# Kernel tuning notes

Measured on AMD Instinct MI355X. Metric: run time of the kernel, lower is better.

The kernel has to match this reference:

```python
import jax, jax.numpy as jnp
import numpy as np

B, S = 16, 4096
E_ENC, E_DEC, H = 1024, 1024, 512


def setup_inputs() -> dict:
    key = jax.random.key(0)
    ks = jax.random.split(key, 8)
    sc_e = 1.0 / np.sqrt(E_ENC)
    sc_d = 1.0 / np.sqrt(E_DEC)
    sc_h = 1.0 / np.sqrt(H)
    return {
        "encoder_hiddens": jax.random.normal(ks[0], (B, S, E_ENC), jnp.float32),
        "decoder_hidden": jax.random.normal(ks[1], (B, E_DEC), jnp.float32),
        "We": jax.random.uniform(ks[2], (E_ENC, H), jnp.float32, -sc_e, sc_e),
        "be": jax.random.uniform(ks[3], (H,), jnp.float32, -sc_e, sc_e),
        "Wd": jax.random.uniform(ks[4], (E_DEC, H), jnp.float32, -sc_d, sc_d),
        "bd": jax.random.uniform(ks[5], (H,), jnp.float32, -sc_d, sc_d),
        "Wo": jax.random.uniform(ks[6], (H, 1), jnp.float32, -sc_h, sc_h),
        "bo": jax.random.uniform(ks[7], (1,), jnp.float32, -sc_h, sc_h),
    }


def reference(encoder_hiddens, decoder_hidden, We, be, Wd, bd, Wo, bo):
    # Additive (Bahdanau) attention.
    # enc_proj: [B,S,H]; dec_proj: [B,1,H] broadcast over sequence.
    enc_proj = jnp.einsum("bse,eh->bsh", encoder_hiddens, We) + be
    dec_proj = jnp.einsum("bd,dh->bh", decoder_hidden, Wd) + bd
    e = jnp.tanh(enc_proj + dec_proj[:, None, :])          # [B,S,H]
    scores = jnp.einsum("bsh,h->bs", e, Wo[:, 0]) + bo[0]  # [B,S]
    attn = jax.nn.softmax(scores, axis=-1)                 # [B,S]
    context = jnp.einsum("bs,bse->be", attn, encoder_hiddens)  # [B,E_ENC]
    return context
```

## Files before the change

### kernel.cpp

```cpp
#include <hip/hip_runtime.h>
#include <hip/hip_bf16.h>
#include <math.h>

#define B_ 16
#define S_ 4096
#define E_ 1024
#define H_ 512

#define BM 128
#define BN 128
#define BK 64
#define NCHUNK (E_ / BK)

typedef short bf16x8 __attribute__((ext_vector_type(8)));
typedef unsigned short u16x8 __attribute__((ext_vector_type(8)));
typedef float f32x4 __attribute__((ext_vector_type(4)));

__device__ inline unsigned short f2bf(float x) {
    __hip_bfloat16 h = __float2bfloat16(x);
    return *(unsigned short*)&h;
}
__device__ inline float bf2f(unsigned short u) {
    unsigned int x = ((unsigned int)u) << 16;
    float f;
    __builtin_memcpy(&f, &x, 4);
    return f;
}
__device__ __forceinline__ void gld16(const unsigned short* g, unsigned short* l) {
    __builtin_amdgcn_global_load_lds(
        (const __attribute__((address_space(1))) void*)g,
        (__attribute__((address_space(3))) void*)l, 16, 0, 0);
}

__global__ __launch_bounds__(256) void prep_conv_kernel(
    const float* __restrict__ enc, const float* __restrict__ We,
    const float* __restrict__ dec, const float* __restrict__ Wd,
    const float* __restrict__ bd, const float* __restrict__ be,
    unsigned short* __restrict__ WeTcB, float* __restrict__ dp,
    unsigned short* __restrict__ encB) {
    __shared__ float red[4][64];
    int bid = blockIdx.x, t = threadIdx.x;
    if (bid < 64) {
        int c = bid >> 2, n0t = (bid & 3) * 128;
#pragma unroll 4
        for (int it = 0; it < 32; ++it) {
            int o = it * 256 + t;
            int n_rel = o >> 6, within = o & 63;
            int cp = within >> 3, j = within & 7;
            int n = n0t + n_rel;
            int k = c * 64 + ((cp ^ (n & 7)) << 3) + j;
            WeTcB[c * 32768 + n * 64 + within] = f2bf(We[(size_t)k * H_ + n]);
        }
    } else if (bid < 192) {
        int id = bid - 64;
        int b = id >> 3, hc = id & 7;
        int h = hc * 64 + (t & 63);
        int ec = t >> 6;
        const float* dr = dec + b * E_ + ec * 256;
        const float* wp = Wd + (size_t)(ec * 256) * H_ + h;
        float acc = 0.f;
#pragma unroll 8
        for (int e = 0; e < 256; ++e) acc = fmaf(dr[e], wp[(size_t)e * H_], acc);
        red[ec][t & 63] = acc;
        __syncthreads();
        if (t < 64) {
            int hh = hc * 64 + t;
            dp[b * H_ + hh] = red[0][t] + red[1][t] + red[2][t] + red[3][t] + bd[hh] + be[hh];
        }
    } else {
        size_t base = ((size_t)(bid - 192) * 256 + t) * 16;
        const float* ep = enc + base;
        unsigned short* op = encB + base;
        float4 v0 = *(const float4*)(ep);
        float4 v1 = *(const float4*)(ep + 4);
        float4 v2 = *(const float4*)(ep + 8);
        float4 v3 = *(const float4*)(ep + 12);
        u16x8 u0, u1;
        u0[0] = f2bf(v0.x); u0[1] = f2bf(v0.y); u0[2] = f2bf(v0.z); u0[3] = f2bf(v0.w);
        u0[4] = f2bf(v1.x); u0[5] = f2bf(v1.y); u0[6] = f2bf(v1.z); u0[7] = f2bf(v1.w);
        u1[0] = f2bf(v2.x); u1[1] = f2bf(v2.y); u1[2] = f2bf(v2.z); u1[3] = f2bf(v2.w);
        u1[4] = f2bf(v3.x); u1[5] = f2bf(v3.y); u1[6] = f2bf(v3.z); u1[7] = f2bf(v3.w);
        *(u16x8*)(op) = u0;
        *(u16x8*)(op + 8) = u1;
    }
}

__global__ __launch_bounds__(256, 3) void scores_gemm_kernel(
    const unsigned short* __restrict__ encB, const unsigned short* __restrict__ WeTcB,
    const float* __restrict__ Wo, const float* __restrict__ dp,
    float* __restrict__ parts) {
    __shared__ unsigned short sA[BM * BK];
    __shared__ unsigned short sB[BN * BK];
    __shared__ float sRed[2][BM];

    int tid = threadIdx.x;
    int w = tid >> 6, l = tid & 63;
    int l16 = l & 15, quad = l >> 4;
    int wm = w & 1, wn = w >> 1;
    int bid = blockIdx.x;
    int xcd = bid & 7;
    int sq = bid >> 3;
    int nt = sq & 3;
    size_t mt = (size_t)((sq >> 2) << 3) + xcd;
    size_t m0 = mt * BM;
    int n0 = nt * BN;
    int b = (int)(m0 >> 12);

    int lrow = l >> 3, lcp = l & 7;
    int qa = lcp ^ (lrow & 7);
    const unsigned short* gA = encB + (m0 + w * 8 + lrow) * E_ + qa * 8;
    const unsigned short* gB = WeTcB + (size_t)n0 * BK + (w * 8) * BK + l * 8;
    unsigned short* sAb = sA + (w * 8) * BK;
    unsigned short* sBb = sB + (w * 8) * BK;

    f32x4 acc[4][4];
#pragma unroll
    for (int i = 0; i < 4; ++i)
#pragma unroll
        for (int j = 0; j < 4; ++j) acc[i][j] = (f32x4)0.f;

    int arow = (wm * 64 + l16) * BK;
    int brow = (wn * 64 + l16) * BK;
    int sw = l16 & 7;

    for (int c = 0; c < NCHUNK; ++c) {
        __syncthreads();
        int k0 = c * BK;
#pragma unroll
        for (int i = 0; i < 4; ++i) {
            gld16(gA + (size_t)i * 32 * E_ + k0, sAb + i * 32 * BK);
            gld16(gB + (size_t)c * (H_ * BK) + i * 32 * BK, sBb + i * 32 * BK);
        }
        __syncthreads();
#pragma unroll
        for (int half = 0; half < 2; ++half) {
            int koff = (((half * 4 + quad) ^ sw) << 3);
            bf16x8 aR[4], bR[4];
#pragma unroll
            for (int i = 0; i < 4; ++i)
                aR[i] = *(const bf16x8*)(sA + arow + i * 16 * BK + koff);
#pragma unroll
            for (int j = 0; j < 4; ++j)
                bR[j] = *(const bf16x8*)(sB + brow + j * 16 * BK + koff);
#pragma unroll
            for (int i = 0; i < 4; ++i)
#pragma unroll
                for (int j = 0; j < 4; ++j)
                    acc[i][j] = __builtin_amdgcn_mfma_f32_16x16x32_bf16(aR[i], bR[j], acc[i][j], 0, 0, 0);
        }
    }

    float dpv[4], wov[4];
    const float* dpb = dp + b * H_;
#pragma unroll
    for (int j = 0; j < 4; ++j) {
        int h = n0 + wn * 64 + j * 16 + l16;
        dpv[j] = dpb[h];
        wov[j] = Wo[h];
    }
#pragma unroll
    for (int i = 0; i < 4; ++i)
#pragma unroll
        for (int r = 0; r < 4; ++r) {
            float s = 0.f;
#pragma unroll
            for (int j = 0; j < 4; ++j) {
                float x = acc[i][j][r] + dpv[j];
                float e = __expf(2.f * x);
                s += (1.f - 2.f / (e + 1.f)) * wov[j];
            }
            s += __shfl_xor(s, 1, 64);
            s += __shfl_xor(s, 2, 64);
            s += __shfl_xor(s, 4, 64);
            s += __shfl_xor(s, 8, 64);
            if (l16 == 0) sRed[wn][wm * 64 + i * 16 + quad * 4 + r] = s;
        }
    __syncthreads();
    if (tid < BM) {
        int s_in = (int)(m0 & (S_ - 1)) + tid;
        parts[(size_t)(nt * B_ + b) * S_ + s_in] = sRed[0][tid] + sRed[1][tid];
    }
}

__global__ __launch_bounds__(256) void stats_kernel(const float* __restrict__ parts,
                                                    float2* __restrict__ stats) {
    int b = blockIdx.x, tid = threadIdx.x;
    const float4* p0 = (const float4*)(parts + (size_t)(0 * B_ + b) * S_);
    const float4* p1 = (const float4*)(parts + (size_t)(1 * B_ + b) * S_);
    const float4* p2 = (const float4*)(parts + (size_t)(2 * B_ + b) * S_);
    const float4* p3 = (const float4*)(parts + (size_t)(3 * B_ + b) * S_);
    float4 v[4];
    float m = -1e30f;
#pragma unroll
    for (int i = 0; i < 4; ++i) {
        int idx = i * 256 + tid;
        float4 a0 = p0[idx], a1 = p1[idx], a2 = p2[idx], a3 = p3[idx];
        v[i].x = a0.x + a1.x + a2.x + a3.x;
        v[i].y = a0.y + a1.y + a2.y + a3.y;
        v[i].z = a0.z + a1.z + a2.z + a3.z;
        v[i].w = a0.w + a1.w + a2.w + a3.w;
        m = fmaxf(m, fmaxf(fmaxf(v[i].x, v[i].y), fmaxf(v[i].z, v[i].w)));
    }
    for (int off = 32; off; off >>= 1) m = fmaxf(m, __shfl_xor(m, off, 64));
    __shared__ float redm[4];
    __shared__ float reds[4];
    if ((tid & 63) == 0) redm[tid >> 6] = m;
    __syncthreads();
    m = fmaxf(fmaxf(redm[0], redm[1]), fmaxf(redm[2], redm[3]));
    float s = 0.f;
#pragma unroll
    for (int i = 0; i < 4; ++i) {
        s += __expf(v[i].x - m) + __expf(v[i].y - m);
        s += __expf(v[i].z - m) + __expf(v[i].w - m);
    }
    for (int off = 32; off; off >>= 1) s += __shfl_xor(s, off, 64);
    if ((tid & 63) == 0) reds[tid >> 6] = s;
    __syncthreads();
    if (tid == 0) {
        stats[b] = make_float2(m, reds[0] + reds[1] + reds[2] + reds[3]);
    }
}

__global__ __launch_bounds__(256) void ctx_partial_bf16(
    const unsigned short* __restrict__ encB, const float* __restrict__ parts,
    const float2* __restrict__ stats, float* __restrict__ part) {
    int b = blockIdx.x >> 5;
    int c = blockIdx.x & 31;
    int s0 = c * 128;
    int tid = threadIdx.x;
    __shared__ float w[128];
    if (tid < 128) {
        size_t idx = (size_t)b * S_ + s0 + tid;
        float x = parts[(size_t)(0 * B_) * S_ + idx] + parts[(size_t)(1 * B_) * S_ + idx] +
                  parts[(size_t)(2 * B_) * S_ + idx] + parts[(size_t)(3 * B_) * S_ + idx];
        w[tid] = __expf(x - stats[b].x);
    }
    __syncthreads();
    int e8 = (tid & 127) * 8;
    int sh = tid >> 7;
    const unsigned short* base = encB + ((size_t)b * S_ + s0 + sh * 64) * E_ + e8;
    const float* wp = w + sh * 64;
    float acc[8];
#pragma unroll
    for (int t = 0; t < 8; ++t) acc[t] = 0.f;
    for (int s = 0; s < 64; s += 8) {
        u16x8 v[8];
#pragma unroll
        for (int u = 0; u < 8; ++u) v[u] = *(const u16x8*)(base + (size_t)(s + u) * E_);
#pragma unroll
        for (int u = 0; u < 8; ++u) {
            float ws = wp[s + u];
#pragma unroll
            for (int t = 0; t < 8; ++t) acc[t] = fmaf(ws, bf2f(v[u][t]), acc[t]);
        }
    }
    float* po = part + ((size_t)(b * 64 + c * 2 + sh)) * E_ + e8;
    *(float4*)(po) = make_float4(acc[0], acc[1], acc[2], acc[3]);
    *(float4*)(po + 4) = make_float4(acc[4], acc[5], acc[6], acc[7]);
}

__global__ __launch_bounds__(256) void ctx_reduce(const float* __restrict__ part,
                                                  const float2* __restrict__ stats,
                                                  float* __restrict__ out) {
    int idx = blockIdx.x * 256 + threadIdx.x;
    int b = idx >> 10;
    int e = idx & 1023;
    const float* p = part + (size_t)b * 64 * E_ + e;
    float s0 = 0.f, s1 = 0.f, s2 = 0.f, s3 = 0.f;
    for (int c = 0; c < 64; c += 4) {
        s0 += p[(size_t)(c + 0) * E_];
        s1 += p[(size_t)(c + 1) * E_];
        s2 += p[(size_t)(c + 2) * E_];
        s3 += p[(size_t)(c + 3) * E_];
    }
    out[idx] = ((s0 + s1) + (s2 + s3)) * (1.f / stats[b].y);
}

extern "C" void kernel_launch(void* const* d_in, const int* in_sizes, int n_in,
                              void* d_out, int out_size, void* d_ws, size_t ws_size,
                              hipStream_t stream) {
    const float* enc = (const float*)d_in[0];
    const float* dec = (const float*)d_in[1];
    const float* We  = (const float*)d_in[2];
    const float* be  = (const float*)d_in[3];
    const float* Wd  = (const float*)d_in[4];
    const float* bd  = (const float*)d_in[5];
    const float* Wo  = (const float*)d_in[6];
    float* out = (float*)d_out;

    char* wsp = (char*)d_ws;
    unsigned short* WeTcB = (unsigned short*)wsp;
    float* dp = (float*)(wsp + (1 << 20));
    float2* stats = (float2*)(wsp + (1 << 20) + (32 << 10));
    float* parts = (float*)(wsp + (1 << 20) + (64 << 10));
    float* part = (float*)(wsp + (4 << 20));
    unsigned short* encB = (unsigned short*)(wsp + (8 << 20));

    prep_conv_kernel<<<192 + 16384, 256, 0, stream>>>(enc, We, dec, Wd, bd, be,
                                                      WeTcB, dp, encB);
    scores_gemm_kernel<<<(B_ * S_ / BM) * (H_ / BN), 256, 0, stream>>>(
        encB, WeTcB, Wo, dp, parts);
    stats_kernel<<<B_, 256, 0, stream>>>(parts, stats);
    ctx_partial_bf16<<<B_ * 32, 256, 0, stream>>>(encB, parts, stats, part);
    ctx_reduce<<<B_ * E_ / 256, 256, 0, stream>>>(part, stats, out);
}
```

Measured before the change: 485.9 us.

## Enlarge score GEMM tiles to 256x256 with double-buffered, staged LDS pipeline

The scores GEMM moves from 128x128 tiles with 4 waves to 256x256 tiles with 8 waves per block. LDS is double-buffered, and the A/B global-to-LDS loads for future K chunks are interleaved between MFMA phases, gated by explicit vmcnt waits, raw barriers and setprio. With 256-wide H tiles only two partial score planes remain, so the stats and context kernels now sum two partials instead of four. The aim is more data reuse per LDS byte and overlap of load latency with MFMA work. The cost is about 128KB of LDS per block, which limits occupancy, plus fragile hand-tuned wait counts.

```diff
diff --git a/kernel.cpp b/kernel.cpp
--- a/kernel.cpp
+++ b/kernel.cpp
@@ -7,8 +7,8 @@
 #define E_ 1024
 #define H_ 512
 
-#define BM 128
-#define BN 128
+#define BM 256
+#define BN 256
 #define BK 64
 #define NCHUNK (E_ / BK)
 
@@ -26,11 +26,14 @@
     __builtin_memcpy(&f, &x, 4);
     return f;
 }
-__device__ __forceinline__ void gld16(const unsigned short* g, unsigned short* l) {
-    __builtin_amdgcn_global_load_lds(
-        (const __attribute__((address_space(1))) void*)g,
-        (__attribute__((address_space(3))) void*)l, 16, 0, 0);
-}
+
+#define GLD16(g, l_) __builtin_amdgcn_global_load_lds(                     \
+    (const __attribute__((address_space(1))) void*)(g),                    \
+    (__attribute__((address_space(3))) void*)(l_), 16, 0, 0)
+
+#define BAR() do { asm volatile("" ::: "memory");                          \
+                   __builtin_amdgcn_s_barrier();                           \
+                   asm volatile("" ::: "memory"); } while (0)
 
 __global__ __launch_bounds__(256) void prep_conv_kernel(
     const float* __restrict__ enc, const float* __restrict__ We,
@@ -85,100 +88,178 @@
     }
 }
 
-__global__ __launch_bounds__(256, 3) void scores_gemm_kernel(
+__global__ __launch_bounds__(512, 2) void scores_gemm_kernel(
     const unsigned short* __restrict__ encB, const unsigned short* __restrict__ WeTcB,
     const float* __restrict__ Wo, const float* __restrict__ dp,
     float* __restrict__ parts) {
-    __shared__ unsigned short sA[BM * BK];
-    __shared__ unsigned short sB[BN * BK];
-    __shared__ float sRed[2][BM];
+    __shared__ unsigned short sA[2][BM * BK];
+    __shared__ unsigned short sB[2][BN * BK];
+    __shared__ float sRed[4][BM];
 
     int tid = threadIdx.x;
-    int w = tid >> 6, l = tid & 63;
+    int w8 = tid >> 6, l = tid & 63;
     int l16 = l & 15, quad = l >> 4;
-    int wm = w & 1, wn = w >> 1;
+    int wm = w8 >> 2, wn = w8 & 3;
+    int lrow = l >> 3, lcp = l & 7;
+
     int bid = blockIdx.x;
     int xcd = bid & 7;
     int sq = bid >> 3;
-    int nt = sq & 3;
-    size_t mt = (size_t)((sq >> 2) << 3) + xcd;
-    size_t m0 = mt * BM;
+    int nt = sq & 1;
+    int mt = ((sq >> 1) << 3) + xcd;
+    size_t m0 = (size_t)mt * BM;
     int n0 = nt * BN;
-    int b = (int)(m0 >> 12);
-
-    int lrow = l >> 3, lcp = l & 7;
-    int qa = lcp ^ (lrow & 7);
-    const unsigned short* gA = encB + (m0 + w * 8 + lrow) * E_ + qa * 8;
-    const unsigned short* gB = WeTcB + (size_t)n0 * BK + (w * 8) * BK + l * 8;
-    unsigned short* sAb = sA + (w * 8) * BK;
-    unsigned short* sBb = sB + (w * 8) * BK;
-
-    f32x4 acc[4][4];
-#pragma unroll
-    for (int i = 0; i < 4; ++i)
+    int b = mt >> 4;
+
+    const unsigned short* gA_base = encB + (m0 + (size_t)(w8 * 8 + lrow)) * E_ + (lcp ^ lrow) * 8;
+    const unsigned short* gB_base = WeTcB + (size_t)(n0 + w8 * 8) * BK + l * 8;
+
+#define STAGE_A(bb, tt, hh) do {                                               \
+        const unsigned short* _s = gA_base + (size_t)((hh) * 128) * E_ + (tt) * BK; \
+        GLD16(_s, &sA[bb][((hh) * 128 + w8 * 8) * BK]);                        \
+        GLD16(_s + (size_t)64 * E_, &sA[bb][((hh) * 128 + 64 + w8 * 8) * BK]); \
+    } while (0)
+#define STAGE_B(bb, tt, hh) do {                                               \
+        const unsigned short* _s = gB_base + (size_t)(tt) * (H_ * BK) + (hh) * 128 * BK; \
+        GLD16(_s, &sB[bb][((hh) * 128 + w8 * 8) * BK]);                        \
+        GLD16(_s + 64 * BK, &sB[bb][((hh) * 128 + 64 + w8 * 8) * BK]);         \
+    } while (0)
+
+    f32x4 acc[8][4];
+#pragma unroll
+    for (int i = 0; i < 8; ++i)
 #pragma unroll
         for (int j = 0; j < 4; ++j) acc[i][j] = (f32x4)0.f;
 
-    int arow = (wm * 64 + l16) * BK;
-    int brow = (wn * 64 + l16) * BK;
+    int aOff = (wm * 128 + l16) * BK;
+    int bOff = (wn * 64 + l16) * BK;
     int sw = l16 & 7;
-
-    for (int c = 0; c < NCHUNK; ++c) {
-        __syncthreads();
-        int k0 = c * BK;
-#pragma unroll
-        for (int i = 0; i < 4; ++i) {
-            gld16(gA + (size_t)i * 32 * E_ + k0, sAb + i * 32 * BK);
-            gld16(gB + (size_t)c * (H_ * BK) + i * 32 * BK, sBb + i * 32 * BK);
-        }
-        __syncthreads();
-#pragma unroll
-        for (int half = 0; half < 2; ++half) {
-            int koff = (((half * 4 + quad) ^ sw) << 3);
-            bf16x8 aR[4], bR[4];
-#pragma unroll
-            for (int i = 0; i < 4; ++i)
-                aR[i] = *(const bf16x8*)(sA + arow + i * 16 * BK + koff);
-#pragma unroll
-            for (int j = 0; j < 4; ++j)
-                bR[j] = *(const bf16x8*)(sB + brow + j * 16 * BK + koff);
-#pragma unroll
-            for (int i = 0; i < 4; ++i)
-#pragma unroll
-                for (int j = 0; j < 4; ++j)
-                    acc[i][j] = __builtin_amdgcn_mfma_f32_16x16x32_bf16(aR[i], bR[j], acc[i][j], 0, 0, 0);
-        }
-    }
+    int kq0 = ((quad ^ sw) << 3);
+    int kq1 = (((4 + quad) ^ sw) << 3);
+
+    STAGE_A(0, 0, 0); STAGE_A(0, 0, 1); STAGE_B(0, 0, 0); STAGE_B(0, 0, 1);
+    STAGE_B(1, 1, 0); STAGE_A(1, 1, 0); STAGE_A(1, 1, 1);
+    asm volatile("s_waitcnt vmcnt(6)" ::: "memory");
+    BAR();
+
+    for (int t = 0; t < NCHUNK; ++t) {
+        int cur = t & 1, nxt = cur ^ 1;
+        const unsigned short* sAc = sA[cur];
+        const unsigned short* sBc = sB[cur];
+        bf16x8 aF[4][2], bF[4][2];
+
+#pragma unroll
+        for (int im = 0; im < 4; ++im) {
+            aF[im][0] = *(const bf16x8*)(sAc + aOff + im * 1024 + kq0);
+            aF[im][1] = *(const bf16x8*)(sAc + aOff + im * 1024 + kq1);
+        }
+#pragma unroll
+        for (int jn = 0; jn < 2; ++jn) {
+            bF[jn][0] = *(const bf16x8*)(sBc + bOff + jn * 1024 + kq0);
+            bF[jn][1] = *(const bf16x8*)(sBc + bOff + jn * 1024 + kq1);
+        }
+        if (t + 1 < NCHUNK) STAGE_B(nxt, t + 1, 1);
+        BAR();
+        __builtin_amdgcn_s_setprio(1);
+#pragma unroll
+        for (int ks = 0; ks < 2; ++ks)
+#pragma unroll
+            for (int im = 0; im < 4; ++im)
+#pragma unroll
+                for (int jn = 0; jn < 2; ++jn)
+                    acc[im][jn] = __builtin_amdgcn_mfma_f32_16x16x32_bf16(
+                        aF[im][ks], bF[jn][ks], acc[im][jn], 0, 0, 0);
+        __builtin_amdgcn_s_setprio(0);
+        BAR();
+
+#pragma unroll
+        for (int jn = 0; jn < 2; ++jn) {
+            bF[2 + jn][0] = *(const bf16x8*)(sBc + bOff + (2 + jn) * 1024 + kq0);
+            bF[2 + jn][1] = *(const bf16x8*)(sBc + bOff + (2 + jn) * 1024 + kq1);
+        }
+        BAR();
+        __builtin_amdgcn_s_setprio(1);
+#pragma unroll
+        for (int ks = 0; ks < 2; ++ks)
+#pragma unroll
+            for (int im = 0; im < 4; ++im)
+#pragma unroll
+                for (int jn = 0; jn < 2; ++jn)
+                    acc[im][2 + jn] = __builtin_amdgcn_mfma_f32_16x16x32_bf16(
+                        aF[im][ks], bF[2 + jn][ks], acc[im][2 + jn], 0, 0, 0);
+        __builtin_amdgcn_s_setprio(0);
+        BAR();
+
+#pragma unroll
+        for (int im = 0; im < 4; ++im) {
+            aF[im][0] = *(const bf16x8*)(sAc + aOff + (4 + im) * 1024 + kq0);
+            aF[im][1] = *(const bf16x8*)(sAc + aOff + (4 + im) * 1024 + kq1);
+        }
+        if (t + 2 < NCHUNK) STAGE_B(cur, t + 2, 0);
+        BAR();
+        __builtin_amdgcn_s_setprio(1);
+#pragma unroll
+        for (int ks = 0; ks < 2; ++ks)
+#pragma unroll
+            for (int im = 0; im < 4; ++im)
+#pragma unroll
+                for (int jn = 0; jn < 2; ++jn)
+                    acc[4 + im][jn] = __builtin_amdgcn_mfma_f32_16x16x32_bf16(
+                        aF[im][ks], bF[jn][ks], acc[4 + im][jn], 0, 0, 0);
+        __builtin_amdgcn_s_setprio(0);
+        BAR();
+
+        if (t + 2 < NCHUNK) { STAGE_A(cur, t + 2, 0); STAGE_A(cur, t + 2, 1); }
+        __builtin_amdgcn_s_setprio(1);
+#pragma unroll
+        for (int ks = 0; ks < 2; ++ks)
+#pragma unroll
+            for (int im = 0; im < 4; ++im)
+#pragma unroll
+                for (int jn = 0; jn < 2; ++jn)
+                    acc[4 + im][2 + jn] = __builtin_amdgcn_mfma_f32_16x16x32_bf16(
+                        aF[im][ks], bF[2 + jn][ks], acc[4 + im][2 + jn], 0, 0, 0);
+        __builtin_amdgcn_s_setprio(0);
+        if (t < NCHUNK - 2) {
+            asm volatile("s_waitcnt vmcnt(6)" ::: "memory");
+        } else if (t == NCHUNK - 2) {
+            asm volatile("s_waitcnt vmcnt(0)" ::: "memory");
+        }
+        if (t < NCHUNK - 1) BAR();
+    }
+#undef STAGE_A
+#undef STAGE_B
 
     float dpv[4], wov[4];
     const float* dpb = dp + b * H_;
 #pragma unroll
-    for (int j = 0; j < 4; ++j) {
-        int h = n0 + wn * 64 + j * 16 + l16;
-        dpv[j] = dpb[h];
-        wov[j] = Wo[h];
-    }
-#pragma unroll
-    for (int i = 0; i < 4; ++i)
+    for (int jn = 0; jn < 4; ++jn) {
+        int h = n0 + wn * 64 + jn * 16 + l16;
+        dpv[jn] = dpb[h];
+        wov[jn] = Wo[h];
+    }
+#pragma unroll
+    for (int im = 0; im < 8; ++im)
 #pragma unroll
         for (int r = 0; r < 4; ++r) {
             float s = 0.f;
 #pragma unroll
-            for (int j = 0; j < 4; ++j) {
-                float x = acc[i][j][r] + dpv[j];
+            for (int jn = 0; jn < 4; ++jn) {
+                float x = acc[im][jn][r] + dpv[jn];
                 float e = __expf(2.f * x);
-                s += (1.f - 2.f / (e + 1.f)) * wov[j];
+                s += (1.f - 2.f / (e + 1.f)) * wov[jn];
             }
             s += __shfl_xor(s, 1, 64);
             s += __shfl_xor(s, 2, 64);
             s += __shfl_xor(s, 4, 64);
             s += __shfl_xor(s, 8, 64);
-            if (l16 == 0) sRed[wn][wm * 64 + i * 16 + quad * 4 + r] = s;
+            if (l16 == 0) sRed[wn][wm * 128 + im * 16 + quad * 4 + r] = s;
         }
     __syncthreads();
     if (tid < BM) {
         int s_in = (int)(m0 & (S_ - 1)) + tid;
-        parts[(size_t)(nt * B_ + b) * S_ + s_in] = sRed[0][tid] + sRed[1][tid];
+        parts[(size_t)(nt * B_ + b) * S_ + s_in] =
+            sRed[0][tid] + sRed[1][tid] + sRed[2][tid] + sRed[3][tid];
     }
 }
 
@@ -187,18 +268,16 @@
     int b = blockIdx.x, tid = threadIdx.x;
     const float4* p0 = (const float4*)(parts + (size_t)(0 * B_ + b) * S_);
     const float4* p1 = (const float4*)(parts + (size_t)(1 * B_ + b) * S_);
-    const float4* p2 = (const float4*)(parts + (size_t)(2 * B_ + b) * S_);
-    const float4* p3 = (const float4*)(parts + (size_t)(3 * B_ + b) * S_);
     float4 v[4];
     float m = -1e30f;
 #pragma unroll
     for (int i = 0; i < 4; ++i) {
         int idx = i * 256 + tid;
-        float4 a0 = p0[idx], a1 = p1[idx], a2 = p2[idx], a3 = p3[idx];
-        v[i].x = a0.x + a1.x + a2.x + a3.x;
-        v[i].y = a0.y + a1.y + a2.y + a3.y;
-        v[i].z = a0.z + a1.z + a2.z + a3.z;
-        v[i].w = a0.w + a1.w + a2.w + a3.w;
+        float4 a0 = p0[idx], a1 = p1[idx];
+        v[i].x = a0.x + a1.x;
+        v[i].y = a0.y + a1.y;
+        v[i].z = a0.z + a1.z;
+        v[i].w = a0.w + a1.w;
         m = fmaxf(m, fmaxf(fmaxf(v[i].x, v[i].y), fmaxf(v[i].z, v[i].w)));
     }
     for (int off = 32; off; off >>= 1) m = fmaxf(m, __shfl_xor(m, off, 64));
@@ -231,8 +310,7 @@
     __shared__ float w[128];
     if (tid < 128) {
         size_t idx = (size_t)b * S_ + s0 + tid;
-        float x = parts[(size_t)(0 * B_) * S_ + idx] + parts[(size_t)(1 * B_) * S_ + idx] +
-                  parts[(size_t)(2 * B_) * S_ + idx] + parts[(size_t)(3 * B_) * S_ + idx];
+        float x = parts[idx] + parts[(size_t)B_ * S_ + idx];
         w[tid] = __expf(x - stats[b].x);
     }
     __syncthreads();
@@ -298,7 +376,7 @@
 
     prep_conv_kernel<<<192 + 16384, 256, 0, stream>>>(enc, We, dec, Wd, bd, be,
                                                       WeTcB, dp, encB);
-    scores_gemm_kernel<<<(B_ * S_ / BM) * (H_ / BN), 256, 0, stream>>>(
+    scores_gemm_kernel<<<(B_ * S_ / BM) * (H_ / BN), 512, 0, stream>>>(
         encB, WeTcB, Wo, dp, parts);
     stats_kernel<<<B_, 256, 0, stream>>>(parts, stats);
     ctx_partial_bf16<<<B_ * 32, 256, 0, stream>>>(encB, parts, stats, part);
```

Result: no change. 489.2 us (+0.7%).

## Fuse fp32-to-bf16 encoder conversion into GEMM loads with double-buffered LDS

Applied to the files above, without the earlier changes.

Removes the separate pass that converted encoder_hiddens to bf16. The scores GEMM now loads fp32 rows into registers, converts them, and writes them to a double-buffered LDS tile, prefetching the next chunk while MFMAs run. The context kernel reads the fp32 encoder directly. This cuts a full write and re-read of a bf16 copy, but each GEMM N-tile now re-reads twice the bytes, and occupancy drops to 2 blocks per CU.

```diff
diff --git a/kernel.cpp b/kernel.cpp
--- a/kernel.cpp
+++ b/kernel.cpp
@@ -20,24 +20,16 @@
     __hip_bfloat16 h = __float2bfloat16(x);
     return *(unsigned short*)&h;
 }
-__device__ inline float bf2f(unsigned short u) {
-    unsigned int x = ((unsigned int)u) << 16;
-    float f;
-    __builtin_memcpy(&f, &x, 4);
-    return f;
-}
-__device__ __forceinline__ void gld16(const unsigned short* g, unsigned short* l) {
-    __builtin_amdgcn_global_load_lds(
-        (const __attribute__((address_space(1))) void*)g,
-        (__attribute__((address_space(3))) void*)l, 16, 0, 0);
-}
-
-__global__ __launch_bounds__(256) void prep_conv_kernel(
-    const float* __restrict__ enc, const float* __restrict__ We,
-    const float* __restrict__ dec, const float* __restrict__ Wd,
-    const float* __restrict__ bd, const float* __restrict__ be,
-    unsigned short* __restrict__ WeTcB, float* __restrict__ dp,
-    unsigned short* __restrict__ encB) {
+
+#define GLD16(g, l_) __builtin_amdgcn_global_load_lds(                     \
+    (const __attribute__((address_space(1))) void*)(g),                    \
+    (__attribute__((address_space(3))) void*)(l_), 16, 0, 0)
+
+__global__ __launch_bounds__(256) void prep_kernel(
+    const float* __restrict__ We, const float* __restrict__ dec,
+    const float* __restrict__ Wd, const float* __restrict__ bd,
+    const float* __restrict__ be, unsigned short* __restrict__ WeTcB,
+    float* __restrict__ dp) {
     __shared__ float red[4][64];
     int bid = blockIdx.x, t = threadIdx.x;
     if (bid < 64) {
@@ -51,7 +43,7 @@
             int k = c * 64 + ((cp ^ (n & 7)) << 3) + j;
             WeTcB[c * 32768 + n * 64 + within] = f2bf(We[(size_t)k * H_ + n]);
         }
-    } else if (bid < 192) {
+    } else {
         int id = bid - 64;
         int b = id >> 3, hc = id & 7;
         int h = hc * 64 + (t & 63);
@@ -67,51 +59,63 @@
             int hh = hc * 64 + t;
             dp[b * H_ + hh] = red[0][t] + red[1][t] + red[2][t] + red[3][t] + bd[hh] + be[hh];
         }
-    } else {
-        size_t base = ((size_t)(bid - 192) * 256 + t) * 16;
-        const float* ep = enc + base;
-        unsigned short* op = encB + base;
-        float4 v0 = *(const float4*)(ep);
-        float4 v1 = *(const float4*)(ep + 4);
-        float4 v2 = *(const float4*)(ep + 8);
-        float4 v3 = *(const float4*)(ep + 12);
-        u16x8 u0, u1;
-        u0[0] = f2bf(v0.x); u0[1] = f2bf(v0.y); u0[2] = f2bf(v0.z); u0[3] = f2bf(v0.w);
-        u0[4] = f2bf(v1.x); u0[5] = f2bf(v1.y); u0[6] = f2bf(v1.z); u0[7] = f2bf(v1.w);
-        u1[0] = f2bf(v2.x); u1[1] = f2bf(v2.y); u1[2] = f2bf(v2.z); u1[3] = f2bf(v2.w);
-        u1[4] = f2bf(v3.x); u1[5] = f2bf(v3.y); u1[6] = f2bf(v3.z); u1[7] = f2bf(v3.w);
-        *(u16x8*)(op) = u0;
-        *(u16x8*)(op + 8) = u1;
-    }
-}
-
-__global__ __launch_bounds__(256, 3) void scores_gemm_kernel(
-    const unsigned short* __restrict__ encB, const unsigned short* __restrict__ WeTcB,
+    }
+}
+
+__global__ __launch_bounds__(256, 2) void scores_gemm_kernel(
+    const float* __restrict__ enc, const unsigned short* __restrict__ WeTcB,
     const float* __restrict__ Wo, const float* __restrict__ dp,
     float* __restrict__ parts) {
-    __shared__ unsigned short sA[BM * BK];
-    __shared__ unsigned short sB[BN * BK];
+    __shared__ unsigned short sA[2][BM * BK];
+    __shared__ unsigned short sB[2][BN * BK];
     __shared__ float sRed[2][BM];
 
     int tid = threadIdx.x;
     int w = tid >> 6, l = tid & 63;
     int l16 = l & 15, quad = l >> 4;
     int wm = w & 1, wn = w >> 1;
+    int lrow = l >> 3, lcp = l & 7;
+
     int bid = blockIdx.x;
     int xcd = bid & 7;
     int sq = bid >> 3;
     int nt = sq & 3;
-    size_t mt = (size_t)((sq >> 2) << 3) + xcd;
-    size_t m0 = mt * BM;
+    int mt = ((sq >> 2) << 3) + xcd;
+    size_t m0 = (size_t)mt * BM;
     int n0 = nt * BN;
-    int b = (int)(m0 >> 12);
-
-    int lrow = l >> 3, lcp = l & 7;
-    int qa = lcp ^ (lrow & 7);
-    const unsigned short* gA = encB + (m0 + w * 8 + lrow) * E_ + qa * 8;
+    int b = mt >> 5;
+
+    const float* gA = enc + (m0 + (size_t)(w * 8 + lrow)) * E_ + lcp * 8;
     const unsigned short* gB = WeTcB + (size_t)n0 * BK + (w * 8) * BK + l * 8;
-    unsigned short* sAb = sA + (w * 8) * BK;
-    unsigned short* sBb = sB + (w * 8) * BK;
+    int awOff = (w * 8 + lrow) * BK + ((lcp ^ lrow) << 3);
+    unsigned short* sBb0 = &sB[0][(w * 8) * BK];
+    unsigned short* sBb1 = &sB[1][(w * 8) * BK];
+
+#define STAGE_B(bb, tt) do {                                                   \
+        const unsigned short* _s = gB + (size_t)(tt) * (H_ * BK);              \
+        unsigned short* _d = (bb) ? sBb1 : sBb0;                               \
+        _Pragma("unroll")                                                      \
+        for (int i = 0; i < 4; ++i) GLD16(_s + i * 32 * BK, _d + i * 32 * BK); \
+    } while (0)
+#define ISSUE_A(tt) do {                                                       \
+        const float* _p = gA + (tt) * BK;                                      \
+        _Pragma("unroll")                                                      \
+        for (int g = 0; g < 4; ++g) {                                          \
+            av[2 * g]     = *(const float4*)(_p + (size_t)(g * 32) * E_);      \
+            av[2 * g + 1] = *(const float4*)(_p + (size_t)(g * 32) * E_ + 4);  \
+        }                                                                      \
+    } while (0)
+#define WRITE_A(bb) do {                                                       \
+        _Pragma("unroll")                                                      \
+        for (int g = 0; g < 4; ++g) {                                          \
+            u16x8 _u;                                                          \
+            _u[0] = f2bf(av[2 * g].x);     _u[1] = f2bf(av[2 * g].y);          \
+            _u[2] = f2bf(av[2 * g].z);     _u[3] = f2bf(av[2 * g].w);          \
+            _u[4] = f2bf(av[2 * g + 1].x); _u[5] = f2bf(av[2 * g + 1].y);      \
+            _u[6] = f2bf(av[2 * g + 1].z); _u[7] = f2bf(av[2 * g + 1].w);      \
+            *(u16x8*)(&sA[bb][awOff + g * 32 * BK]) = _u;                      \
+        }                                                                      \
+    } while (0)
 
     f32x4 acc[4][4];
 #pragma unroll
@@ -123,32 +127,44 @@
     int brow = (wn * 64 + l16) * BK;
     int sw = l16 & 7;
 
-    for (int c = 0; c < NCHUNK; ++c) {
-        __syncthreads();
-        int k0 = c * BK;
-#pragma unroll
-        for (int i = 0; i < 4; ++i) {
-            gld16(gA + (size_t)i * 32 * E_ + k0, sAb + i * 32 * BK);
-            gld16(gB + (size_t)c * (H_ * BK) + i * 32 * BK, sBb + i * 32 * BK);
-        }
-        __syncthreads();
+    float4 av[8];
+    STAGE_B(0, 0);
+    ISSUE_A(0);
+    WRITE_A(0);
+    __syncthreads();
+
+    for (int t = 0; t < NCHUNK; ++t) {
+        int cur = t & 1, nxt = cur ^ 1;
+        const unsigned short* sAc = sA[cur];
+        const unsigned short* sBc = sB[cur];
+
+        if (t + 1 < NCHUNK) {
+            STAGE_B(nxt, t + 1);
+            ISSUE_A(t + 1);
+        }
 #pragma unroll
         for (int half = 0; half < 2; ++half) {
             int koff = (((half * 4 + quad) ^ sw) << 3);
             bf16x8 aR[4], bR[4];
 #pragma unroll
             for (int i = 0; i < 4; ++i)
-                aR[i] = *(const bf16x8*)(sA + arow + i * 16 * BK + koff);
+                aR[i] = *(const bf16x8*)(sAc + arow + i * 16 * BK + koff);
 #pragma unroll
             for (int j = 0; j < 4; ++j)
-                bR[j] = *(const bf16x8*)(sB + brow + j * 16 * BK + koff);
+                bR[j] = *(const bf16x8*)(sBc + brow + j * 16 * BK + koff);
 #pragma unroll
             for (int i = 0; i < 4; ++i)
 #pragma unroll
                 for (int j = 0; j < 4; ++j)
-                    acc[i][j] = __builtin_amdgcn_mfma_f32_16x16x32_bf16(aR[i], bR[j], acc[i][j], 0, 0, 0);
-        }
-    }
+                    acc[i][j] = __builtin_amdgcn_mfma_f32_16x16x32_bf16(
+                        aR[i], bR[j], acc[i][j], 0, 0, 0);
+        }
+        if (t + 1 < NCHUNK) WRITE_A(nxt);
+        __syncthreads();
+    }
+#undef STAGE_B
+#undef ISSUE_A
+#undef WRITE_A
 
     float dpv[4], wov[4];
     const float* dpb = dp + b * H_;
@@ -221,8 +237,8 @@
     }
 }
 
-__global__ __launch_bounds__(256) void ctx_partial_bf16(
-    const unsigned short* __restrict__ encB, const float* __restrict__ parts,
+__global__ __launch_bounds__(256) void ctx_partial_f32(
+    const float* __restrict__ enc, const float* __restrict__ parts,
     const float2* __restrict__ stats, float* __restrict__ part) {
     int b = blockIdx.x >> 5;
     int c = blockIdx.x & 31;
@@ -231,27 +247,36 @@
     __shared__ float w[128];
     if (tid < 128) {
         size_t idx = (size_t)b * S_ + s0 + tid;
-        float x = parts[(size_t)(0 * B_) * S_ + idx] + parts[(size_t)(1 * B_) * S_ + idx] +
+        float x = parts[idx] + parts[(size_t)B_ * S_ + idx] +
                   parts[(size_t)(2 * B_) * S_ + idx] + parts[(size_t)(3 * B_) * S_ + idx];
         w[tid] = __expf(x - stats[b].x);
     }
     __syncthreads();
     int e8 = (tid & 127) * 8;
     int sh = tid >> 7;
-    const unsigned short* base = encB + ((size_t)b * S_ + s0 + sh * 64) * E_ + e8;
+    const float* base = enc + ((size_t)b * S_ + s0 + sh * 64) * E_ + e8;
     const float* wp = w + sh * 64;
     float acc[8];
 #pragma unroll
     for (int t = 0; t < 8; ++t) acc[t] = 0.f;
-    for (int s = 0; s < 64; s += 8) {
-        u16x8 v[8];
-#pragma unroll
-        for (int u = 0; u < 8; ++u) v[u] = *(const u16x8*)(base + (size_t)(s + u) * E_);
-#pragma unroll
-        for (int u = 0; u < 8; ++u) {
+    for (int s = 0; s < 64; s += 4) {
+        float4 v0[4], v1[4];
+#pragma unroll
+        for (int u = 0; u < 4; ++u) {
+            v0[u] = *(const float4*)(base + (size_t)(s + u) * E_);
+            v1[u] = *(const float4*)(base + (size_t)(s + u) * E_ + 4);
+        }
+#pragma unroll
+        for (int u = 0; u < 4; ++u) {
             float ws = wp[s + u];
-#pragma unroll
-            for (int t = 0; t < 8; ++t) acc[t] = fmaf(ws, bf2f(v[u][t]), acc[t]);
+            acc[0] = fmaf(ws, v0[u].x, acc[0]);
+            acc[1] = fmaf(ws, v0[u].y, acc[1]);
+            acc[2] = fmaf(ws, v0[u].z, acc[2]);
+            acc[3] = fmaf(ws, v0[u].w, acc[3]);
+            acc[4] = fmaf(ws, v1[u].x, acc[4]);
+            acc[5] = fmaf(ws, v1[u].y, acc[5]);
+            acc[6] = fmaf(ws, v1[u].z, acc[6]);
+            acc[7] = fmaf(ws, v1[u].w, acc[7]);
         }
     }
     float* po = part + ((size_t)(b * 64 + c * 2 + sh)) * E_ + e8;
@@ -294,13 +319,11 @@
     float2* stats = (float2*)(wsp + (1 << 20) + (32 << 10));
     float* parts = (float*)(wsp + (1 << 20) + (64 << 10));
     float* part = (float*)(wsp + (4 << 20));
-    unsigned short* encB = (unsigned short*)(wsp + (8 << 20));
-
-    prep_conv_kernel<<<192 + 16384, 256, 0, stream>>>(enc, We, dec, Wd, bd, be,
-                                                      WeTcB, dp, encB);
+
+    prep_kernel<<<192, 256, 0, stream>>>(We, dec, Wd, bd, be, WeTcB, dp);
     scores_gemm_kernel<<<(B_ * S_ / BM) * (H_ / BN), 256, 0, stream>>>(
-        encB, WeTcB, Wo, dp, parts);
+        enc, WeTcB, Wo, dp, parts);
     stats_kernel<<<B_, 256, 0, stream>>>(parts, stats);
-    ctx_partial_bf16<<<B_ * 32, 256, 0, stream>>>(encB, parts, stats, part);
+    ctx_partial_f32<<<B_ * 32, 256, 0, stream>>>(enc, parts, stats, part);
     ctx_reduce<<<B_ * E_ / 256, 256, 0, stream>>>(part, stats, out);
 }
```

Result: slower. 558.5 us (+15.0%).

## Widen scores GEMM tile to BN=256 and double-buffer A tiles

Applied to the files above, without the earlier changes.

The scores GEMM tile width grows from 128 to 256 columns, so H splits into 2 tiles instead of 4. This halves how often each encoder row block is reloaded and halves the partial-score buffers that the stats and context kernels must sum. A software pipeline double-buffers the A tile in LDS and prefetches the next chunk during MFMA, with raised wave priority around the compute. The cost is more accumulator registers (occupancy hint drops from 3 to 2 blocks), extra barriers for reloading the single-buffered B tile, and fewer blocks in the grid.

```diff
diff --git a/kernel.cpp b/kernel.cpp
--- a/kernel.cpp
+++ b/kernel.cpp
@@ -8,7 +8,7 @@
 #define H_ 512
 
 #define BM 128
-#define BN 128
+#define BN 256
 #define BK 64
 #define NCHUNK (E_ / BK)
 
@@ -85,11 +85,11 @@
     }
 }
 
-__global__ __launch_bounds__(256, 3) void scores_gemm_kernel(
+__global__ __launch_bounds__(256, 2) void scores_gemm_kernel(
     const unsigned short* __restrict__ encB, const unsigned short* __restrict__ WeTcB,
     const float* __restrict__ Wo, const float* __restrict__ dp,
     float* __restrict__ parts) {
-    __shared__ unsigned short sA[BM * BK];
+    __shared__ unsigned short sA[2][BM * BK];
     __shared__ unsigned short sB[BN * BK];
     __shared__ float sRed[2][BM];
 
@@ -97,64 +97,96 @@
     int w = tid >> 6, l = tid & 63;
     int l16 = l & 15, quad = l >> 4;
     int wm = w & 1, wn = w >> 1;
+    int lrow = l >> 3, lcp = l & 7;
+
     int bid = blockIdx.x;
     int xcd = bid & 7;
     int sq = bid >> 3;
-    int nt = sq & 3;
-    size_t mt = (size_t)((sq >> 2) << 3) + xcd;
-    size_t m0 = mt * BM;
+    int nt = sq & 1;
+    int mt = ((sq >> 1) << 3) + xcd;
+    size_t m0 = (size_t)mt * BM;
     int n0 = nt * BN;
-    int b = (int)(m0 >> 12);
-
-    int lrow = l >> 3, lcp = l & 7;
-    int qa = lcp ^ (lrow & 7);
-    const unsigned short* gA = encB + (m0 + w * 8 + lrow) * E_ + qa * 8;
+    int b = mt >> 5;
+
+    const unsigned short* gA = encB + (m0 + (size_t)(w * 8 + lrow)) * E_ + (lcp ^ lrow) * 8;
     const unsigned short* gB = WeTcB + (size_t)n0 * BK + (w * 8) * BK + l * 8;
-    unsigned short* sAb = sA + (w * 8) * BK;
-    unsigned short* sBb = sB + (w * 8) * BK;
-
-    f32x4 acc[4][4];
+    unsigned short* sAb0 = &sA[0][(w * 8) * BK];
+    unsigned short* sAb1 = &sA[1][(w * 8) * BK];
+    unsigned short* sBb = &sB[(w * 8) * BK];
+
+#define STAGE_A(bb, tt) do {                                                   \
+        const unsigned short* _s = gA + (tt) * BK;                             \
+        unsigned short* _d = (bb) ? sAb1 : sAb0;                               \
+        _Pragma("unroll")                                                      \
+        for (int i = 0; i < 4; ++i)                                            \
+            gld16(_s + (size_t)(i * 32) * E_, _d + i * 32 * BK);               \
+    } while (0)
+#define STAGE_B(tt) do {                                                       \
+        const unsigned short* _s = gB + (size_t)(tt) * (H_ * BK);              \
+        _Pragma("unroll")                                                      \
+        for (int i = 0; i < 8; ++i) gld16(_s + i * 32 * BK, sBb + i * 32 * BK);\
+    } while (0)
+
+    f32x4 acc[4][8];
 #pragma unroll
     for (int i = 0; i < 4; ++i)
 #pragma unroll
-        for (int j = 0; j < 4; ++j) acc[i][j] = (f32x4)0.f;
+        for (int j = 0; j < 8; ++j) acc[i][j] = (f32x4)0.f;
 
     int arow = (wm * 64 + l16) * BK;
-    int brow = (wn * 64 + l16) * BK;
+    int brow = (wn * 128 + l16) * BK;
     int sw = l16 & 7;
 
-    for (int c = 0; c < NCHUNK; ++c) {
-        __syncthreads();
-        int k0 = c * BK;
-#pragma unroll
-        for (int i = 0; i < 4; ++i) {
-            gld16(gA + (size_t)i * 32 * E_ + k0, sAb + i * 32 * BK);
-            gld16(gB + (size_t)c * (H_ * BK) + i * 32 * BK, sBb + i * 32 * BK);
-        }
-        __syncthreads();
+    STAGE_B(0);
+    STAGE_A(0, 0);
+    asm volatile("s_waitcnt vmcnt(0) lgkmcnt(0)" ::: "memory");
+    __builtin_amdgcn_s_barrier();
+    asm volatile("" ::: "memory");
+
+    for (int t = 0; t < NCHUNK; ++t) {
+        int cur = t & 1, nxt = cur ^ 1;
+        const unsigned short* sAc = sA[cur];
+
+        if (t + 1 < NCHUNK) STAGE_A(nxt, t + 1);
+
+        __builtin_amdgcn_s_setprio(1);
 #pragma unroll
         for (int half = 0; half < 2; ++half) {
             int koff = (((half * 4 + quad) ^ sw) << 3);
-            bf16x8 aR[4], bR[4];
+            bf16x8 aR[4], bR[8];
 #pragma unroll
             for (int i = 0; i < 4; ++i)
-                aR[i] = *(const bf16x8*)(sA + arow + i * 16 * BK + koff);
-#pragma unroll
-            for (int j = 0; j < 4; ++j)
+                aR[i] = *(const bf16x8*)(sAc + arow + i * 16 * BK + koff);
+#pragma unroll
+            for (int j = 0; j < 8; ++j)
                 bR[j] = *(const bf16x8*)(sB + brow + j * 16 * BK + koff);
 #pragma unroll
             for (int i = 0; i < 4; ++i)
 #pragma unroll
-                for (int j = 0; j < 4; ++j)
-                    acc[i][j] = __builtin_amdgcn_mfma_f32_16x16x32_bf16(aR[i], bR[j], acc[i][j], 0, 0, 0);
-        }
-    }
-
-    float dpv[4], wov[4];
+                for (int j = 0; j < 8; ++j)
+                    acc[i][j] = __builtin_amdgcn_mfma_f32_16x16x32_bf16(
+                        aR[i], bR[j], acc[i][j], 0, 0, 0);
+        }
+        __builtin_amdgcn_s_setprio(0);
+
+        if (t + 1 < NCHUNK) {
+            asm volatile("s_waitcnt lgkmcnt(0)" ::: "memory");
+            __builtin_amdgcn_s_barrier();
+            asm volatile("" ::: "memory");
+            STAGE_B(t + 1);
+            asm volatile("s_waitcnt vmcnt(0)" ::: "memory");
+            __builtin_amdgcn_s_barrier();
+            asm volatile("" ::: "memory");
+        }
+    }
+#undef STAGE_A
+#undef STAGE_B
+
+    float dpv[8], wov[8];
     const float* dpb = dp + b * H_;
 #pragma unroll
-    for (int j = 0; j < 4; ++j) {
-        int h = n0 + wn * 64 + j * 16 + l16;
+    for (int j = 0; j < 8; ++j) {
+        int h = n0 + wn * 128 + j * 16 + l16;
         dpv[j] = dpb[h];
         wov[j] = Wo[h];
     }
@@ -164,7 +196,7 @@
         for (int r = 0; r < 4; ++r) {
             float s = 0.f;
 #pragma unroll
-            for (int j = 0; j < 4; ++j) {
+            for (int j = 0; j < 8; ++j) {
                 float x = acc[i][j][r] + dpv[j];
                 float e = __expf(2.f * x);
                 s += (1.f - 2.f / (e + 1.f)) * wov[j];
@@ -187,18 +219,16 @@
     int b = blockIdx.x, tid = threadIdx.x;
     const float4* p0 = (const float4*)(parts + (size_t)(0 * B_ + b) * S_);
     const float4* p1 = (const float4*)(parts + (size_t)(1 * B_ + b) * S_);
-    const float4* p2 = (const float4*)(parts + (size_t)(2 * B_ + b) * S_);
-    const float4* p3 = (const float4*)(parts + (size_t)(3 * B_ + b) * S_);
     float4 v[4];
     float m = -1e30f;
 #pragma unroll
     for (int i = 0; i < 4; ++i) {
         int idx = i * 256 + tid;
-        float4 a0 = p0[idx], a1 = p1[idx], a2 = p2[idx], a3 = p3[idx];
-        v[i].x = a0.x + a1.x + a2.x + a3.x;
-        v[i].y = a0.y + a1.y + a2.y + a3.y;
-        v[i].z = a0.z + a1.z + a2.z + a3.z;
-        v[i].w = a0.w + a1.w + a2.w + a3.w;
+        float4 a0 = p0[idx], a1 = p1[idx];
+        v[i].x = a0.x + a1.x;
+        v[i].y = a0.y + a1.y;
+        v[i].z = a0.z + a1.z;
+        v[i].w = a0.w + a1.w;
         m = fmaxf(m, fmaxf(fmaxf(v[i].x, v[i].y), fmaxf(v[i].z, v[i].w)));
     }
     for (int off = 32; off; off >>= 1) m = fmaxf(m, __shfl_xor(m, off, 64));
@@ -231,8 +261,7 @@
     __shared__ float w[128];
     if (tid < 128) {
         size_t idx = (size_t)b * S_ + s0 + tid;
-        float x = parts[(size_t)(0 * B_) * S_ + idx] + parts[(size_t)(1 * B_) * S_ + idx] +
-                  parts[(size_t)(2 * B_) * S_ + idx] + parts[(size_t)(3 * B_) * S_ + idx];
+        float x = parts[idx] + parts[(size_t)B_ * S_ + idx];
         w[tid] = __expf(x - stats[b].x);
     }
     __syncthreads();
```

Result: no change. 490.9 us (+1.0%).
